# Optimization experiments

Hardware: AMD Instinct MI355X
Metric: run time of the kernel (lower is better)

## Reference

```python
import jax, jax.numpy as jnp
import numpy as np

CLIP_MIN = 0.0
CLIP_MAX = 1.0
B, T, F, E, CD = 64, 48, 128, 64, 32


def setup_inputs() -> dict:
    key = jax.random.key(0)
    ks = jax.random.split(key, 8)
    return {
        "input_x": jax.random.uniform(ks[0], (B, T, F), dtype=jnp.float32),
        "mask": jax.random.randint(ks[1], (B, T, F), 0, 2, dtype=jnp.int32),
        "embed0": jax.random.normal(ks[2], (F, E), dtype=jnp.float32) * 0.1,
        "embed1": jax.random.normal(ks[3], (F, E), dtype=jnp.float32) * 0.1,
        "embed_missing": jax.random.normal(ks[4], (F, E), dtype=jnp.float32) * 0.1,
        "attention_f_w": jax.random.normal(ks[5], (F, E), dtype=jnp.float32) * 0.1,
        "attention_f_b": jnp.zeros((F,), dtype=jnp.float32),
        "compress_w": jax.random.normal(ks[6], (2 * E, CD), dtype=jnp.float32) * 0.1,
    }


def reference(input_x, mask, embed0, embed1, embed_missing, attention_f_w, attention_f_b, compress_w):
    b, t, f = input_x.shape
    # new_mask: feature observed anywhere in time -> [b, 1, f, 1] (broadcasts over time)
    m = (jnp.sum(mask, axis=-2) != 0).astype(input_x.dtype)[:, None, :, None]
    x = input_x[..., None]  # [b, t, f, 1]
    # interval embedding c: [b, t, f, e]
    c0 = (x - m * CLIP_MIN) * embed0
    c1 = (m * CLIP_MAX - x) * embed1
    c = (c0 + c1) / (CLIP_MAX - CLIP_MIN) + (1.0 - m) * embed_missing
    # pairwise scores: sum_e c_i * c_j * w_i + b_i  (avoids [b,t,f,f,e] materialization)
    scores = jnp.einsum("btie,btje->btij", c * attention_f_w, c) + attention_f_b[:, None]
    scores = jnp.clip(scores, -5.0, 5.0)
    off_diag = 1.0 - jnp.eye(f, dtype=c.dtype)
    masked_exps = jnp.exp(scores) * off_diag
    attn = masked_exps / (jnp.sum(masked_exps, axis=-1, keepdims=True) + 1e-8)  # [b,t,f,f]
    # weighted aggregation: sum_j attn_ij * (c_i * c_j) = c_i * (attn @ c)_i
    agg = c * jnp.einsum("btij,btje->btie", attn, c)
    a = jax.nn.relu(jnp.concatenate([c, agg], axis=-1))  # [b,t,f,2e]
    out = jnp.einsum("btfk,kd->btfd", a, compress_w)
    return out.reshape(b, t, f * compress_w.shape[-1])
```

## Files before the change

### kernel.cpp

```cpp
#include <hip/hip_runtime.h>

#define NB 64
#define NT 48
#define NF 128
#define NE 64
#define NCD 32

#define LOG2E 1.4426950408889634f

typedef __attribute__((ext_vector_type(8))) short bf16x8;
typedef __attribute__((ext_vector_type(4))) float f32x4;
typedef __attribute__((ext_vector_type(2))) uint u32x2;

#define WS_MFLAG 0
#define WS_DB    32768
#define WS_E1B   49152
#define WS_EMB   65536
#define WS_WLB   81920
#define WS_WT    98304
#define WS_BL    106496

__device__ __forceinline__ ushort f2bf(float x) {
    union { float f; uint u; } v; v.f = x;
    uint r = v.u + 0x7fffu + ((v.u >> 16) & 1u);
    return (ushort)(r >> 16);
}
__device__ __forceinline__ uint pk_bf16(float lo, float hi) {
    uint r; asm("v_cvt_pk_bf16_f32 %0, %1, %2" : "=v"(r) : "v"(lo), "v"(hi)); return r;
}
__device__ __forceinline__ float bflo(uint u) { union { uint u; float f; } v; v.u = u << 16; return v.f; }
__device__ __forceinline__ float bfhi(uint u) { union { uint u; float f; } v; v.u = u & 0xffff0000u; return v.f; }
__device__ __forceinline__ float exp2i(float x) { float r; asm("v_exp_f32 %0, %1" : "=v"(r) : "v"(x)); return r; }
__device__ __forceinline__ float rcpi(float x)  { float r; asm("v_rcp_f32 %0, %1" : "=v"(r) : "v"(x)); return r; }

#define TRR(dst, addr, IMM) \
    asm volatile("ds_read_b64_tr_b16 %0, %1 offset:" IMM : "=v"(dst) : "v"(addr))
#define PLSWAP(a, b) asm("v_permlane32_swap_b32 %0, %1" : "+v"(a), "+v"(b))

#define AGG_ISSUE(CR, TB, O0, O1, O2, O3, O4, O5, O6, O7) \
    TRR(CR[0], TB, O0); TRR(CR[1], TB, O1); \
    TRR(CR[2], TB, O2); TRR(CR[3], TB, O3); \
    TRR(CR[4], TB, O4); TRR(CR[5], TB, O5); \
    TRR(CR[6], TB, O6); TRR(CR[7], TB, O7); \
    __builtin_amdgcn_sched_barrier(0);

#define AGG_CONSUME(CR, PF, AG) { \
    union { u32x2 d[2]; bf16x8 v; } q0, q1, q2, q3; \
    q0.d[0] = CR[0]; q0.d[1] = CR[1]; q1.d[0] = CR[2]; q1.d[1] = CR[3]; \
    q2.d[0] = CR[4]; q2.d[1] = CR[5]; q3.d[0] = CR[6]; q3.d[1] = CR[7]; \
    AG[0] = __builtin_amdgcn_mfma_f32_16x16x32_bf16(q0.v, PF, AG[0], 0, 0, 0); \
    AG[1] = __builtin_amdgcn_mfma_f32_16x16x32_bf16(q1.v, PF, AG[1], 0, 0, 0); \
    AG[2] = __builtin_amdgcn_mfma_f32_16x16x32_bf16(q2.v, PF, AG[2], 0, 0, 0); \
    AG[3] = __builtin_amdgcn_mfma_f32_16x16x32_bf16(q3.v, PF, AG[3], 0, 0, 0); }

#define PF_BUILD(PF, PP, KS) { \
    uint X0 = PP[4*(KS)], X1 = PP[4*(KS)+1], X2 = PP[4*(KS)+2], X3 = PP[4*(KS)+3]; \
    PLSWAP(X0, X2); PLSWAP(X1, X3); \
    PF.u[0] = X0; PF.u[1] = X1; PF.u[2] = X2; PF.u[3] = X3; }

#define LGKM_WAIT(N) \
    asm volatile("s_waitcnt lgkmcnt(" #N ")" ::: "memory"); \
    __builtin_amdgcn_sched_barrier(0);

__global__ __launch_bounds__(256) void prep_kernel(
    const int* __restrict__ mask, const float* __restrict__ e0, const float* __restrict__ e1,
    const float* __restrict__ em, const float* __restrict__ aw, const float* __restrict__ ab,
    const float* __restrict__ cw,
    uint* __restrict__ mflag, ushort* __restrict__ db, ushort* __restrict__ e1b,
    ushort* __restrict__ emb, ushort* __restrict__ wlb, ushort* __restrict__ wt,
    float* __restrict__ bl)
{
    const int blk = blockIdx.x, tid = threadIdx.x;
    if (blk < 32) {
        int idx = blk * 256 + tid;
        float e1v = e1[idx];
        e1b[idx] = f2bf(e1v);
        emb[idx] = f2bf(em[idx]);
        db[idx]  = f2bf(e0[idx] - e1v);
        wlb[idx] = f2bf(aw[idx] * LOG2E);
    } else if (blk < 64) {
        int idx = (blk - 32) * 256 + tid;
        int b = idx >> 7, f = idx & 127;
        const int* p = mask + b * (NT * NF) + f;
        int s = 0;
#pragma unroll
        for (int t = 0; t < NT; ++t) s += p[t * NF];
        mflag[idx] = (s != 0) ? 1u : 0u;
    } else if (blk < 80) {
        int idx = (blk - 64) * 256 + tid;
        int k = idx >> 5, d = idx & 31;
        int kd;
        if (k < 64) kd = k;
        else {
            int kk = k - 64;
            kd = 64 + ((kk & 51) | ((kk & 4) << 1) | ((kk & 8) >> 1));
        }
        wt[d * 128 + kd] = f2bf(cw[idx]);
    } else {
        if (tid < NF) bl[tid] = ab[tid] * LOG2E;
    }
}

__global__ __launch_bounds__(512, 4) void fused_kernel(
    const float* __restrict__ input_x, const uint* __restrict__ mflag,
    const ushort* __restrict__ db, const ushort* __restrict__ e1b, const ushort* __restrict__ emb,
    const ushort* __restrict__ wlb, const float* __restrict__ blog,
    const ushort* __restrict__ wt, float* __restrict__ out)
{
    __shared__ ushort sC[2 * 9248];

    const int tid = threadIdx.x;
    const int blk = blockIdx.x;
    const int b   = blk / 24;
    const int bt0 = b * NT + (blk % 24) * 2;
    const int bt1 = bt0 + 1;

    const int wv = tid >> 6, ln = tid & 63;
    const int lr = ln & 15, lg = ln >> 4;
    const int i0 = wv << 4, irow = i0 + lr;

    const float bl = blog[irow];
    const float x0 = input_x[bt0 * NF + irow];
    const float x1 = input_x[bt1 * NF + irow];
    const ushort* Mrow = (mflag[b * NF + irow] ? e1b : emb) + irow * NE;
    const ushort* Drow = db + irow * NE;
    const ushort* Wrow = wlb + irow * NE;

    const int sbase = (lg >> 1) * 2312 + (lr >> 2) * 72 + (lr & 3) * 16 + (lg & 1) * 8;

    ushort* sC0 = sC;
    ushort* sC1 = sC + 9248;

    bf16x8 cwf0[2], cwf1[2];
#pragma unroll
    for (int ks = 0; ks < 2; ++ks) {
        const int eo = ks * 32 + lg * 8;
        uint d4[4], m4[4], w4[4];
        *(uint4*)d4 = *(const uint4*)(Drow + eo);
        *(uint4*)m4 = *(const uint4*)(Mrow + eo);
        *(uint4*)w4 = *(const uint4*)(Wrow + eo);
        uint cb0[4], cb1[4];
        union { uint u[4]; bf16x8 v; } cw0, cw1;
#pragma unroll
        for (int j = 0; j < 4; ++j) {
            float dlo = bflo(d4[j]), dhi = bfhi(d4[j]);
            float mlo = bflo(m4[j]), mhi = bfhi(m4[j]);
            float wlo = bflo(w4[j]), whi = bfhi(w4[j]);
            float c0lo = fmaf(x0, dlo, mlo), c0hi = fmaf(x0, dhi, mhi);
            float c1lo = fmaf(x1, dlo, mlo), c1hi = fmaf(x1, dhi, mhi);
            cb0[j] = pk_bf16(c0lo, c0hi);
            cb1[j] = pk_bf16(c1lo, c1hi);
            cw0.u[j] = pk_bf16(c0lo * wlo, c0hi * whi);
            cw1.u[j] = pk_bf16(c1lo * wlo, c1hi * whi);
        }
        cwf0[ks] = cw0.v; cwf1[ks] = cw1.v;
        *(uint4*)&sC0[sbase + wv * 288 + ks * 4624] = *(uint4*)cb0;
        *(uint4*)&sC1[sbase + wv * 288 + ks * 4624] = *(uint4*)cb1;
    }
    __syncthreads();

    auto run_S4 = [&](const ushort* base, bf16x8 w0, bf16x8 w1, int jt0, f32x4* st4) {
#pragma unroll
        for (int j = 0; j < 4; ++j) {
            const int jt = jt0 + j;
            f32x4 a = (f32x4){bl, bl, bl, bl};
            bf16x8 a0 = *(bf16x8*)&base[sbase + jt * 288];
            a = __builtin_amdgcn_mfma_f32_16x16x32_bf16(a0, w0, a, 0, 0, 0);
            bf16x8 a1 = *(bf16x8*)&base[sbase + jt * 288 + 4624];
            a = __builtin_amdgcn_mfma_f32_16x16x32_bf16(a1, w1, a, 0, 0, 0);
            st4[j] = a;
        }
    };
    auto run_SM4 = [&](f32x4* st4, uint* pp, int jt0, float* rsa) {
#pragma unroll
        for (int j = 0; j < 4; ++j) {
            const int jt = jt0 + j;
            f32x4 v = st4[j];
            float e0 = exp2i(v[0]);
            float e1 = exp2i(v[1]);
            float e2 = exp2i(v[2]);
            float e3 = exp2i(v[3]);
            if (jt == wv) {
                const bool on = (lg == (lr >> 2));
                e0 = (on && (lr & 3) == 0) ? 0.f : e0;
                e1 = (on && (lr & 3) == 1) ? 0.f : e1;
                e2 = (on && (lr & 3) == 2) ? 0.f : e2;
                e3 = (on && (lr & 3) == 3) ? 0.f : e3;
            }
            rsa[0] += e0; rsa[1] += e1; rsa[2] += e2; rsa[3] += e3;
            pp[2 * jt]     = pk_bf16(e0, e1);
            pp[2 * jt + 1] = pk_bf16(e2, e3);
        }
    };
    auto run_chainS = [&](const ushort* base, bf16x8 w0, bf16x8 w1, uint* pp) -> float {
        f32x4 st4[4];
        float rsa[4] = {0.f, 0.f, 0.f, 0.f};
        run_S4(base, w0, w1, 0, st4);
        run_SM4(st4, pp, 0, rsa);
        run_S4(base, w0, w1, 4, st4);
        run_SM4(st4, pp, 4, rsa);
        float rs = (rsa[0] + rsa[1]) + (rsa[2] + rsa[3]);
        rs += __shfl_xor(rs, 16);
        rs += __shfl_xor(rs, 32);
        return rcpi(rs + 1e-8f);
    };
    auto run_AGG = [&](const ushort* base, uint* pp, f32x4* ag) {
#pragma unroll
        for (int et = 0; et < 4; ++et) ag[et] = (f32x4){0.f, 0.f, 0.f, 0.f};
        const uint tb = (uint)(uintptr_t)base
                      + 2u * (uint)(72 * (((lg >> 1) << 2) + (lg & 1)) + lr);
        u32x2 cA[8], cB[8];
        union { uint u[4]; bf16x8 v; } pf0, pf1, pf2, pf3;
        LGKM_WAIT(0);
        PF_BUILD(pf0, pp, 0);
        AGG_ISSUE(cA, tb, "0", "144", "4624", "4768", "9248", "9392", "13872", "14016");
        PF_BUILD(pf1, pp, 1);
        AGG_ISSUE(cB, tb, "1152", "1296", "5776", "5920", "10400", "10544", "15024", "15168");
        LGKM_WAIT(8);
        AGG_CONSUME(cA, pf0.v, ag);
        PF_BUILD(pf2, pp, 2);
        AGG_ISSUE(cA, tb, "2304", "2448", "6928", "7072", "11552", "11696", "16176", "16320");
        LGKM_WAIT(8);
        AGG_CONSUME(cB, pf1.v, ag);
        PF_BUILD(pf3, pp, 3);
        AGG_ISSUE(cB, tb, "3456", "3600", "8080", "8224", "12704", "12848", "17328", "17472");
        LGKM_WAIT(8);
        AGG_CONSUME(cA, pf2.v, ag);
        LGKM_WAIT(0);
        AGG_CONSUME(cB, pf3.v, ag);
    };
    auto run_EPI = [&](const ushort* base, f32x4* ag, float inv, uint* aa) {
        const int ebase = (wv * 4 + (lr >> 2)) * 72 + (lr & 3) * 16 + lg * 4;
#pragma unroll
        for (int et = 0; et < 4; ++et) {
            u32x2 cb2 = *(u32x2*)&base[ebase + et * 2312];
            float a0f = fmaxf(ag[et][0] * inv * bflo(cb2.x), 0.f);
            float a1f = fmaxf(ag[et][1] * inv * bfhi(cb2.x), 0.f);
            float a2f = fmaxf(ag[et][2] * inv * bflo(cb2.y), 0.f);
            float a3f = fmaxf(ag[et][3] * inv * bfhi(cb2.y), 0.f);
            aa[2 * et]     = pk_bf16(a0f, a1f);
            aa[2 * et + 1] = pk_bf16(a2f, a3f);
        }
    };
    auto run_OUT = [&](const ushort* base, uint* aa, const bf16x8* wf, int bt) {
        f32x4 oc[2];
        oc[0] = (f32x4){0.f, 0.f, 0.f, 0.f};
        oc[1] = (f32x4){0.f, 0.f, 0.f, 0.f};
#pragma unroll
        for (int ks = 0; ks < 4; ++ks) {
            bf16x8 afr;
            if (ks < 2) {
                const uint4 cc = *(uint4*)&base[sbase + wv * 288 + ks * 4624];
                union { uint u[4]; bf16x8 v; } rl;
                asm("v_pk_max_i16 %0, %1, 0" : "=v"(rl.u[0]) : "v"(cc.x));
                asm("v_pk_max_i16 %0, %1, 0" : "=v"(rl.u[1]) : "v"(cc.y));
                asm("v_pk_max_i16 %0, %1, 0" : "=v"(rl.u[2]) : "v"(cc.z));
                asm("v_pk_max_i16 %0, %1, 0" : "=v"(rl.u[3]) : "v"(cc.w));
                afr = rl.v;
            } else {
                const int kk = ks - 2;
                uint Y0 = aa[4 * kk], Y1 = aa[4 * kk + 1], Y2 = aa[4 * kk + 2], Y3 = aa[4 * kk + 3];
                PLSWAP(Y0, Y2);
                PLSWAP(Y1, Y3);
                union { uint u[4]; bf16x8 v; } af;
                af.u[0] = Y0; af.u[1] = Y1; af.u[2] = Y2; af.u[3] = Y3;
                afr = af.v;
            }
            oc[0] = __builtin_amdgcn_mfma_f32_16x16x32_bf16(afr, wf[ks * 2 + 0], oc[0], 0, 0, 0);
            oc[1] = __builtin_amdgcn_mfma_f32_16x16x32_bf16(afr, wf[ks * 2 + 1], oc[1], 0, 0, 0);
        }
        float* op = out + bt * (NF * NCD);
#pragma unroll
        for (int dt = 0; dt < 2; ++dt)
#pragma unroll
            for (int r = 0; r < 4; ++r)
                op[(i0 + lg * 4 + r) * NCD + dt * 16 + lr] = oc[dt][r];
    };

    uint pp0[16], pp1[16];
    f32x4 ag0[4], ag1[4];
    uint aa0[8], aa1[8];

    const float inv0 = run_chainS(sC0, cwf0[0], cwf0[1], pp0);
    const float inv1 = run_chainS(sC1, cwf1[0], cwf1[1], pp1);

    run_AGG(sC0, pp0, ag0);
    run_EPI(sC0, ag0, inv0, aa0);
    run_AGG(sC1, pp1, ag1);

    bf16x8 wf[8];
#pragma unroll
    for (int ks = 0; ks < 4; ++ks)
#pragma unroll
        for (int dt = 0; dt < 2; ++dt)
            wf[ks * 2 + dt] = *(const bf16x8*)(wt + (dt * 16 + lr) * 128 + ks * 32 + lg * 8);

    run_EPI(sC1, ag1, inv1, aa1);
    run_OUT(sC0, aa0, wf, bt0);
    run_OUT(sC1, aa1, wf, bt1);
}

extern "C" void kernel_launch(void* const* d_in, const int* in_sizes, int n_in,
                              void* d_out, int out_size, void* d_ws, size_t ws_size,
                              hipStream_t stream) {
    const float* input_x       = (const float*)d_in[0];
    const int*   mask          = (const int*)d_in[1];
    const float* embed0        = (const float*)d_in[2];
    const float* embed1        = (const float*)d_in[3];
    const float* embed_missing = (const float*)d_in[4];
    const float* attn_w        = (const float*)d_in[5];
    const float* attn_b        = (const float*)d_in[6];
    const float* compress_w    = (const float*)d_in[7];
    float* out = (float*)d_out;

    char* ws = (char*)d_ws;
    uint*   mflag = (uint*)(ws + WS_MFLAG);
    ushort* dbp   = (ushort*)(ws + WS_DB);
    ushort* e1bp  = (ushort*)(ws + WS_E1B);
    ushort* embp  = (ushort*)(ws + WS_EMB);
    ushort* wlbp  = (ushort*)(ws + WS_WLB);
    ushort* wtp   = (ushort*)(ws + WS_WT);
    float*  blp   = (float*)(ws + WS_BL);

    hipLaunchKernelGGL(prep_kernel, dim3(81), dim3(256), 0, stream,
                       mask, embed0, embed1, embed_missing, attn_w, attn_b, compress_w,
                       mflag, dbp, e1bp, embp, wlbp, wtp, blp);
    hipLaunchKernelGGL(fused_kernel, dim3(NB * NT / 2), dim3(512), 0, stream,
                       input_x, mflag, dbp, e1bp, embp, wlbp, blp, wtp, out);
}
```

Before: 39.34 us.

## Serialize the two timestep chains to cut register pressure and raise occupancy

Processes the two (b,t) slices one after the other instead of interleaving them. This drops the second slice's live arrays (probabilities, aggregation, activations), the double-buffered AGG loads and the preloaded compress weights. Launch bounds go from 4 to 6 waves per EU, and the second slice's c*w fragment is rebuilt from shared memory after the first chain finishes. The cost is less instruction-level overlap between the two chains, serialized LDS waits in the aggregation, a second rounding of c to bf16 before multiplying by w, and compress weights reloaded from global memory inside each chain.

```diff
diff --git a/kernel.cpp b/kernel.cpp
--- a/kernel.cpp
+++ b/kernel.cpp
@@ -101,7 +101,7 @@
     }
 }
 
-__global__ __launch_bounds__(512, 4) void fused_kernel(
+__global__ __launch_bounds__(512, 6) void fused_kernel(
     const float* __restrict__ input_x, const uint* __restrict__ mflag,
     const ushort* __restrict__ db, const ushort* __restrict__ e1b, const ushort* __restrict__ emb,
     const ushort* __restrict__ wlb, const float* __restrict__ blog,
@@ -131,7 +131,7 @@
     ushort* sC0 = sC;
     ushort* sC1 = sC + 9248;
 
-    bf16x8 cwf0[2], cwf1[2];
+    bf16x8 cwf0[2];
 #pragma unroll
     for (int ks = 0; ks < 2; ++ks) {
         const int eo = ks * 32 + lg * 8;
@@ -140,20 +140,18 @@
         *(uint4*)m4 = *(const uint4*)(Mrow + eo);
         *(uint4*)w4 = *(const uint4*)(Wrow + eo);
         uint cb0[4], cb1[4];
-        union { uint u[4]; bf16x8 v; } cw0, cw1;
+        union { uint u[4]; bf16x8 v; } cw0;
 #pragma unroll
         for (int j = 0; j < 4; ++j) {
             float dlo = bflo(d4[j]), dhi = bfhi(d4[j]);
             float mlo = bflo(m4[j]), mhi = bfhi(m4[j]);
-            float wlo = bflo(w4[j]), whi = bfhi(w4[j]);
             float c0lo = fmaf(x0, dlo, mlo), c0hi = fmaf(x0, dhi, mhi);
             float c1lo = fmaf(x1, dlo, mlo), c1hi = fmaf(x1, dhi, mhi);
             cb0[j] = pk_bf16(c0lo, c0hi);
             cb1[j] = pk_bf16(c1lo, c1hi);
-            cw0.u[j] = pk_bf16(c0lo * wlo, c0hi * whi);
-            cw1.u[j] = pk_bf16(c1lo * wlo, c1hi * whi);
-        }
-        cwf0[ks] = cw0.v; cwf1[ks] = cw1.v;
+            cw0.u[j] = pk_bf16(c0lo * bflo(w4[j]), c0hi * bfhi(w4[j]));
+        }
+        cwf0[ks] = cw0.v;
         *(uint4*)&sC0[sbase + wv * 288 + ks * 4624] = *(uint4*)cb0;
         *(uint4*)&sC1[sbase + wv * 288 + ks * 4624] = *(uint4*)cb1;
     }
@@ -192,62 +190,64 @@
             pp[2 * jt + 1] = pk_bf16(e2, e3);
         }
     };
-    auto run_chainS = [&](const ushort* base, bf16x8 w0, bf16x8 w1, uint* pp) -> float {
-        f32x4 st4[4];
-        float rsa[4] = {0.f, 0.f, 0.f, 0.f};
-        run_S4(base, w0, w1, 0, st4);
-        run_SM4(st4, pp, 0, rsa);
-        run_S4(base, w0, w1, 4, st4);
-        run_SM4(st4, pp, 4, rsa);
-        float rs = (rsa[0] + rsa[1]) + (rsa[2] + rsa[3]);
-        rs += __shfl_xor(rs, 16);
-        rs += __shfl_xor(rs, 32);
-        return rcpi(rs + 1e-8f);
-    };
-    auto run_AGG = [&](const ushort* base, uint* pp, f32x4* ag) {
+    auto run_chain = [&](const ushort* base, bf16x8 w0, bf16x8 w1, int bt) {
+        uint pp[16];
+        float inv;
+        {
+            f32x4 st4[4];
+            float rsa[4] = {0.f, 0.f, 0.f, 0.f};
+            run_S4(base, w0, w1, 0, st4);
+            run_SM4(st4, pp, 0, rsa);
+            run_S4(base, w0, w1, 4, st4);
+            run_SM4(st4, pp, 4, rsa);
+            float rs = (rsa[0] + rsa[1]) + (rsa[2] + rsa[3]);
+            rs += __shfl_xor(rs, 16);
+            rs += __shfl_xor(rs, 32);
+            inv = rcpi(rs + 1e-8f);
+        }
+        f32x4 ag[4];
 #pragma unroll
         for (int et = 0; et < 4; ++et) ag[et] = (f32x4){0.f, 0.f, 0.f, 0.f};
-        const uint tb = (uint)(uintptr_t)base
-                      + 2u * (uint)(72 * (((lg >> 1) << 2) + (lg & 1)) + lr);
-        u32x2 cA[8], cB[8];
-        union { uint u[4]; bf16x8 v; } pf0, pf1, pf2, pf3;
-        LGKM_WAIT(0);
-        PF_BUILD(pf0, pp, 0);
-        AGG_ISSUE(cA, tb, "0", "144", "4624", "4768", "9248", "9392", "13872", "14016");
-        PF_BUILD(pf1, pp, 1);
-        AGG_ISSUE(cB, tb, "1152", "1296", "5776", "5920", "10400", "10544", "15024", "15168");
-        LGKM_WAIT(8);
-        AGG_CONSUME(cA, pf0.v, ag);
-        PF_BUILD(pf2, pp, 2);
-        AGG_ISSUE(cA, tb, "2304", "2448", "6928", "7072", "11552", "11696", "16176", "16320");
-        LGKM_WAIT(8);
-        AGG_CONSUME(cB, pf1.v, ag);
-        PF_BUILD(pf3, pp, 3);
-        AGG_ISSUE(cB, tb, "3456", "3600", "8080", "8224", "12704", "12848", "17328", "17472");
-        LGKM_WAIT(8);
-        AGG_CONSUME(cA, pf2.v, ag);
-        LGKM_WAIT(0);
-        AGG_CONSUME(cB, pf3.v, ag);
-    };
-    auto run_EPI = [&](const ushort* base, f32x4* ag, float inv, uint* aa) {
-        const int ebase = (wv * 4 + (lr >> 2)) * 72 + (lr & 3) * 16 + lg * 4;
-#pragma unroll
-        for (int et = 0; et < 4; ++et) {
-            u32x2 cb2 = *(u32x2*)&base[ebase + et * 2312];
-            float a0f = fmaxf(ag[et][0] * inv * bflo(cb2.x), 0.f);
-            float a1f = fmaxf(ag[et][1] * inv * bfhi(cb2.x), 0.f);
-            float a2f = fmaxf(ag[et][2] * inv * bflo(cb2.y), 0.f);
-            float a3f = fmaxf(ag[et][3] * inv * bfhi(cb2.y), 0.f);
-            aa[2 * et]     = pk_bf16(a0f, a1f);
-            aa[2 * et + 1] = pk_bf16(a2f, a3f);
-        }
-    };
-    auto run_OUT = [&](const ushort* base, uint* aa, const bf16x8* wf, int bt) {
+        {
+            const uint tb = (uint)(uintptr_t)base
+                          + 2u * (uint)(72 * (((lg >> 1) << 2) + (lg & 1)) + lr);
+            u32x2 cA[8];
+            union { uint u[4]; bf16x8 v; } pf;
+            LGKM_WAIT(0);
+            PF_BUILD(pf, pp, 0);
+            AGG_ISSUE(cA, tb, "0", "144", "4624", "4768", "9248", "9392", "13872", "14016");
+            LGKM_WAIT(0);  AGG_CONSUME(cA, pf.v, ag);
+            PF_BUILD(pf, pp, 1);
+            AGG_ISSUE(cA, tb, "1152", "1296", "5776", "5920", "10400", "10544", "15024", "15168");
+            LGKM_WAIT(0);  AGG_CONSUME(cA, pf.v, ag);
+            PF_BUILD(pf, pp, 2);
+            AGG_ISSUE(cA, tb, "2304", "2448", "6928", "7072", "11552", "11696", "16176", "16320");
+            LGKM_WAIT(0);  AGG_CONSUME(cA, pf.v, ag);
+            PF_BUILD(pf, pp, 3);
+            AGG_ISSUE(cA, tb, "3456", "3600", "8080", "8224", "12704", "12848", "17328", "17472");
+            LGKM_WAIT(0);  AGG_CONSUME(cA, pf.v, ag);
+        }
+        uint aa[8];
+        {
+            const int ebase = (wv * 4 + (lr >> 2)) * 72 + (lr & 3) * 16 + lg * 4;
+#pragma unroll
+            for (int et = 0; et < 4; ++et) {
+                u32x2 cb2 = *(u32x2*)&base[ebase + et * 2312];
+                float a0f = fmaxf(ag[et][0] * inv * bflo(cb2.x), 0.f);
+                float a1f = fmaxf(ag[et][1] * inv * bfhi(cb2.x), 0.f);
+                float a2f = fmaxf(ag[et][2] * inv * bflo(cb2.y), 0.f);
+                float a3f = fmaxf(ag[et][3] * inv * bfhi(cb2.y), 0.f);
+                aa[2 * et]     = pk_bf16(a0f, a1f);
+                aa[2 * et + 1] = pk_bf16(a2f, a3f);
+            }
+        }
         f32x4 oc[2];
         oc[0] = (f32x4){0.f, 0.f, 0.f, 0.f};
         oc[1] = (f32x4){0.f, 0.f, 0.f, 0.f};
 #pragma unroll
         for (int ks = 0; ks < 4; ++ks) {
+            bf16x8 wfa = *(const bf16x8*)(wt + lr * 128 + ks * 32 + lg * 8);
+            bf16x8 wfb = *(const bf16x8*)(wt + (16 + lr) * 128 + ks * 32 + lg * 8);
             bf16x8 afr;
             if (ks < 2) {
                 const uint4 cc = *(uint4*)&base[sbase + wv * 288 + ks * 4624];
@@ -266,8 +266,8 @@
                 af.u[0] = Y0; af.u[1] = Y1; af.u[2] = Y2; af.u[3] = Y3;
                 afr = af.v;
             }
-            oc[0] = __builtin_amdgcn_mfma_f32_16x16x32_bf16(afr, wf[ks * 2 + 0], oc[0], 0, 0, 0);
-            oc[1] = __builtin_amdgcn_mfma_f32_16x16x32_bf16(afr, wf[ks * 2 + 1], oc[1], 0, 0, 0);
+            oc[0] = __builtin_amdgcn_mfma_f32_16x16x32_bf16(afr, wfa, oc[0], 0, 0, 0);
+            oc[1] = __builtin_amdgcn_mfma_f32_16x16x32_bf16(afr, wfb, oc[1], 0, 0, 0);
         }
         float* op = out + bt * (NF * NCD);
 #pragma unroll
@@ -277,27 +277,23 @@
                 op[(i0 + lg * 4 + r) * NCD + dt * 16 + lr] = oc[dt][r];
     };
 
-    uint pp0[16], pp1[16];
-    f32x4 ag0[4], ag1[4];
-    uint aa0[8], aa1[8];
-
-    const float inv0 = run_chainS(sC0, cwf0[0], cwf0[1], pp0);
-    const float inv1 = run_chainS(sC1, cwf1[0], cwf1[1], pp1);
-
-    run_AGG(sC0, pp0, ag0);
-    run_EPI(sC0, ag0, inv0, aa0);
-    run_AGG(sC1, pp1, ag1);
-
-    bf16x8 wf[8];
-#pragma unroll
-    for (int ks = 0; ks < 4; ++ks)
-#pragma unroll
-        for (int dt = 0; dt < 2; ++dt)
-            wf[ks * 2 + dt] = *(const bf16x8*)(wt + (dt * 16 + lr) * 128 + ks * 32 + lg * 8);
-
-    run_EPI(sC1, ag1, inv1, aa1);
-    run_OUT(sC0, aa0, wf, bt0);
-    run_OUT(sC1, aa1, wf, bt1);
+    run_chain(sC0, cwf0[0], cwf0[1], bt0);
+
+    bf16x8 cwf1[2];
+#pragma unroll
+    for (int ks = 0; ks < 2; ++ks) {
+        bf16x8 cf = *(bf16x8*)&sC1[sbase + wv * 288 + ks * 4624];
+        uint w4[4];
+        *(uint4*)w4 = *(const uint4*)(Wrow + ks * 32 + lg * 8);
+        const uint* cu = (const uint*)&cf;
+        union { uint u[4]; bf16x8 v; } cwu;
+#pragma unroll
+        for (int j = 0; j < 4; ++j)
+            cwu.u[j] = pk_bf16(bflo(cu[j]) * bflo(w4[j]), bfhi(cu[j]) * bfhi(w4[j]));
+        cwf1[ks] = cwu.v;
+    }
+
+    run_chain(sC1, cwf1[0], cwf1[1], bt1);
 }
 
 extern "C" void kernel_launch(void* const* d_in, const int* in_sizes, int n_in,
```

Measured after the change: 48.92 us. 1.24x slower.
